# Performance work log

Hardware: AMD Instinct MI355X
Metric: run time of the kernel (lower is better)

The kernel has to match this reference:

```python
import jax, jax.numpy as jnp
import numpy as np

DIM, FFN, GC, NSET, K = 48, 2, 2, 32, 3
HID = DIM * FFN          # 96 hidden features
G = HID // GC            # 48 groups in KBA
CG = HID // G            # 2 channels per group
INTERC = 24              # min(dim, 24)
B, H, W = 4, 128, 128


def _conv(x, w, b=None, groups=1, pad=0):
    out = jax.lax.conv_general_dilated(
        x, w, (1, 1), [(pad, pad), (pad, pad)],
        dimension_numbers=('NCHW', 'OIHW', 'NCHW'),
        feature_group_count=groups)
    if b is not None:
        out = out + b[None, :, None, None]
    return out


def _kba(x, att, k, g, bb, ww):
    # x: [B,c,H,W], att: [B,nset,H,W], bb: [1,nset,c], ww: [1,nset,c*c//g*k*k]
    Bz, c, Hh, Ww = x.shape
    KK = k * k
    cg = c // g
    P = Hh * Ww
    a = att.reshape(Bz, -1, P).transpose(0, 2, 1)                     # [B,P,nset]
    bias = jnp.einsum('bpn,nc->bpc', a, bb[0])                        # [B,P,c]
    attk = jnp.einsum('bpn,nm->bpm', a, ww[0]).reshape(Bz, P, g, cg, cg * KK)
    pd = k // 2
    xp = jnp.pad(x, ((0, 0), (0, 0), (pd, pd), (pd, pd)))
    # im2col patches, torch.unfold layout: channel-major, kernel row-major
    patches = jnp.stack([xp[:, :, i:i + Hh, j:j + Ww]
                         for i in range(k) for j in range(k)], axis=2)  # [B,c,KK,H,W]
    uf = patches.reshape(Bz, g, cg * KK, P).transpose(0, 3, 1, 2)       # [B,P,g,cg*KK]
    out = jnp.einsum('bpgom,bpgm->bpgo', attk, uf).reshape(Bz, P, c) + bias
    return out.transpose(0, 2, 1).reshape(Bz, c, Hh, Ww)


def setup_inputs() -> dict:
    key = jax.random.key(0)
    ks = jax.random.split(key, 20)
    s = 0.05
    inp = {
        'x': jax.random.normal(ks[0], (B, DIM, H, W), jnp.float32),
        'dw1_w': jax.random.normal(ks[1], (HID, DIM, 1, 1), jnp.float32) * s,
        'dw2_w': jax.random.normal(ks[2], (HID, 1, 3, 3), jnp.float32) * s,
        'proj_w': jax.random.normal(ks[3], (DIM, HID, 1, 1), jnp.float32) * s,
        'sca_w': jax.random.normal(ks[4], (HID, HID, 1, 1), jnp.float32) * s,
        'sca_b': jax.random.normal(ks[5], (HID,), jnp.float32) * s,
        'c1_w1': jax.random.normal(ks[6], (HID, DIM, 1, 1), jnp.float32) * s,
        'c1_w2': jax.random.normal(ks[7], (HID, 1, 3, 3), jnp.float32) * s,
        'kba_w': jax.random.normal(ks[8], (1, NSET, HID * CG * K * K), jnp.float32) * s,
        'kba_b': jax.random.normal(ks[9], (1, NSET, HID), jnp.float32) * s,
        'c2_w1': jax.random.normal(ks[10], (INTERC, DIM // INTERC, 3, 3), jnp.float32) * s,
        'c2_b1': jax.random.normal(ks[11], (INTERC,), jnp.float32) * s,
        'c2_w2': jax.random.normal(ks[12], (NSET, INTERC // 2, 1, 1), jnp.float32) * s,
        'c2_b2': jax.random.normal(ks[13], (NSET,), jnp.float32) * s,
        'c211_w': jax.random.normal(ks[14], (NSET, DIM, 1, 1), jnp.float32) * s,
        'c211_b': jax.random.normal(ks[15], (NSET,), jnp.float32) * s,
        'attgamma': jnp.full((1, NSET, 1, 1), 0.01, jnp.float32),
        'ga1': jnp.full((1, HID, 1, 1), 0.01, jnp.float32),
    }
    return inp


def reference(x, dw1_w, dw2_w, proj_w, sca_w, sca_b, c1_w1, c1_w2,
              kba_w, kba_b, c2_w1, c2_b1, c2_w2, c2_b2,
              c211_w, c211_b, attgamma, ga1):
    # dwconv branch: 1x1 -> depthwise 3x3
    x1 = _conv(_conv(x, dw1_w), dw2_w, groups=HID, pad=1)
    # attention map branch: grouped 3x3 -> SimpleGate -> 1x1, scaled + skip 1x1
    t = _conv(x, c2_w1, c2_b1, groups=INTERC, pad=1)
    t1, t2 = jnp.split(t, 2, axis=1)
    t = _conv(t1 * t2, c2_w2, c2_b2)
    att = t * attgamma + _conv(x, c211_w, c211_b)
    # conv1 branch feeding KBA
    uf = _conv(_conv(x, c1_w1), c1_w2, groups=HID, pad=1)
    x2 = _kba(uf, att, K, G, kba_b, kba_w) * ga1 + uf
    comb = jax.nn.gelu(x1, approximate=False) * x2
    pooled = jnp.mean(comb, axis=(2, 3), keepdims=True)
    comb = comb * _conv(pooled, sca_w, sca_b)
    return _conv(comb, proj_w)
```

## Files before the change

kernel.cpp:

```cpp
#include <hip/hip_runtime.h>
#include <math.h>

#define BB 4
#define HH 128
#define WW 128
#define HWP (HH*WW)
#define DIMC 48
#define HIDC 96
#define NSETC 32

typedef __attribute__((ext_vector_type(8))) short bf16x8;
typedef __attribute__((ext_vector_type(4))) float f32x4;
typedef __attribute__((ext_vector_type(2))) float f32x2;

static __device__ __forceinline__ unsigned short f2bf(float f) {
    union { float f; unsigned u; } v; v.f = f;
    unsigned r = (v.u + 0x7FFFu + ((v.u >> 16) & 1u)) >> 16;
    return (unsigned short)r;
}
static __device__ __forceinline__ unsigned rnd_bf(float f) {
    union { float f; unsigned u; } v; v.f = f;
    return v.u + 0x8000u;
}
static __device__ __forceinline__ unsigned pack2bf(float lo, float hi) {
    return __builtin_amdgcn_perm(rnd_bf(hi), rnd_bf(lo), 0x07060302u);
}
static __device__ __forceinline__ void st_bf_hi(unsigned short* p, float f) {
    *p = (unsigned short)(rnd_bf(f) >> 16);
}
static __device__ __forceinline__ float bf2f(unsigned short u) {
    union { unsigned u; float f; } v; v.u = ((unsigned)u) << 16;
    return v.f;
}
static __device__ __forceinline__ float bfpair_lo(unsigned pr) {
    union { unsigned u; float f; } v; v.u = pr << 16; return v.f;
}
static __device__ __forceinline__ float bfpair_hi(unsigned pr) {
    union { unsigned u; float f; } v; v.u = pr & 0xffff0000u; return v.f;
}
static __device__ __forceinline__ float gelu(float x) {
    return 0.5f * x * (1.0f + erff(x * 0.70710678118654752f));
}

__global__ __launch_bounds__(256) void k_prep(
    const float* __restrict__ x,
    const float* __restrict__ kbaw, const float* __restrict__ kbab,
    const float* __restrict__ dw1w, const float* __restrict__ c1w1,
    const float* __restrict__ ga1,  const float* __restrict__ c211w,
    const float* __restrict__ c2w2, const float* __restrict__ c2b2,
    const float* __restrict__ c211b, const float* __restrict__ attg,
    unsigned short* __restrict__ Bpk, unsigned short* __restrict__ Bpw,
    unsigned short* __restrict__ Aps, unsigned short* __restrict__ Ag,
    unsigned* __restrict__ x_p, float* __restrict__ pooled)
{
    __shared__ unsigned ts[256 * 26];
    int blk = blockIdx.x, tid = threadIdx.x;
    if (blk < 300) {
        int t = blk * 256 + tid;
        if (t < 61440) {
            int j = t & 7, lane = (t >> 3) & 63, tile = t >> 9;
            int chunk = tile / 10, nt = tile - chunk * 10;
            int m = lane & 15, qn = lane >> 4;
            int lc = 4 * nt + (m & 3);
            int o = lc / 20, tt = lc % 20;
            int c = (m >> 2) * 24 + 2 * chunk + o;
            int n = qn * 8 + j;
            float v = 0.f;
            if (tt < 18)       v = kbaw[n * 1728 + (c >> 1) * 36 + (c & 1) * 18 + tt] * ga1[c];
            else if (tt == 18) v = kbab[n * 96 + c] * ga1[c];
            Bpk[t] = f2bf(v);
        } else if (t < 73728) {
            int u = t - 61440;
            int s = u / 6144;
            int rem = u % 6144;
            int nt = rem >> 9;
            int lane = (rem >> 3) & 63, j = rem & 7;
            int k = s * 32 + ((lane >> 4) << 3) + j;
            int col = (nt << 4) + (lane & 15);
            float v = 0.f;
            if (k < 48) v = (col < 96) ? dw1w[col * 48 + k] : c1w1[(col - 96) * 48 + k];
            Bpw[u] = f2bf(v);
        } else if (t < 75776) {
            int u = t - 73728;
            int j = u & 7, lane = (u >> 3) & 63, tile = u >> 9;
            int kt = tile >> 1, nt2 = tile & 1;
            int m = lane & 15, qn = lane >> 4;
            int n = 8 * (m >> 2) + 4 * nt2 + (m & 3);
            int k = kt * 32 + qn * 8 + j;
            Aps[u] = f2bf(k < 48 ? c211w[n * 48 + k] : 0.f);
        } else if (t < 76800) {
            int u = t - 75776;
            int j = u & 7, lane = (u >> 3) & 63, nt2 = u >> 9;
            int m = lane & 15, qn = lane >> 4;
            int n = 8 * (m >> 2) + 4 * nt2 + (m & 3);
            int k = qn * 8 + j;
            float v = 0.f;
            if (k < 12)       v = c2w2[n * 12 + k] * attg[n];
            else if (k == 12) v = c2b2[n] * attg[n] + c211b[n];
            Ag[u] = f2bf(v);
        }
    } else {
        int xblk = blk - 300;
        if (xblk == 0) {
            for (int i = tid; i < BB * HIDC; i += 256) pooled[i] = 0.f;
        }
        int b = xblk >> 6;
        int p0 = (xblk & 63) << 8;
        const float* xb = x + (size_t)b * DIMC * HWP + p0;
        #pragma unroll
        for (int c2 = 0; c2 < 24; ++c2) {
            float lo = xb[(2 * c2) * HWP + tid];
            float hi = xb[(2 * c2 + 1) * HWP + tid];
            ts[tid * 26 + c2] = pack2bf(lo, hi);
        }
        __syncthreads();
        unsigned* dst = x_p + ((size_t)b * HWP + p0) * 24;
        for (int idx = tid; idx < 256 * 24; idx += 256) {
            int px = idx / 24, j2 = idx - px * 24;
            dst[px * 24 + j2] = ts[px * 26 + j2];
        }
    }
}

__global__ __launch_bounds__(256, 2) void k_mff(
    const unsigned* __restrict__ x_p,
    const uint4* __restrict__ BpkA, const uint4* __restrict__ Bpw,
    const uint4* __restrict__ Aps,  const uint4* __restrict__ Ag,
    const float* __restrict__ c1w2, const float* __restrict__ dw2w,
    const float* __restrict__ c2w1, const float* __restrict__ c2b1,
    unsigned* __restrict__ comb_bf, float* __restrict__ pooled)
{
    __shared__ __attribute__((aligned(16))) unsigned xs[144 * 26];
    __shared__ __attribute__((aligned(16))) unsigned short hsw[144 * 100];
    __shared__ unsigned short us2p[100 * 100];
    __shared__ float wls[864 + 432 + 24];
    __shared__ float pooled_s[96];

    int lane = threadIdx.x, wy = threadIdx.y;
    int tid = wy * 64 + lane;
    int blk = blockIdx.x;
    int b = blk >> 8, ty = (blk >> 4) & 15, tx = blk & 15;
    int q = lane >> 4, i16 = lane & 15;

    float* wats  = wls + 864;
    float* c2b1s = wls + 864 + 432;
    float* att_tf = (float*)hsw;

    if (tid < 96) pooled_s[tid] = 0.f;
    for (int idx = tid; idx < 864; idx += 256) {
        int t5 = idx / 96, c = idx - t5 * 96;
        wls[idx] = dw2w[c * 9 + t5];
    }
    for (int idx = tid; idx < 216; idx += 256) {
        int g = idx / 9, tap = idx - g * 9;
        wats[idx * 2]     = c2w1[g * 18 + tap];
        wats[idx * 2 + 1] = c2w1[g * 18 + 9 + tap];
    }
    if (tid < 24) c2b1s[tid] = c2b1[tid];
    for (int idx = tid; idx < 144 * 12; idx += 256) {
        int pos = idx / 12, jp = idx - pos * 12;
        int gy = ty * 8 - 2 + pos / 12, gx = tx * 8 - 2 + pos % 12;
        uint2 v = {0u, 0u};
        if (((unsigned)gy < (unsigned)HH) & ((unsigned)gx < (unsigned)WW))
            v = *(const uint2*)&x_p[((size_t)b * HWP + gy * WW + gx) * 24 + jp * 2];
        *(uint2*)&xs[pos * 26 + jp * 2] = v;
    }
    __syncthreads();

    int p_t = wy * 16 + i16;
    int pyT = p_t >> 3, pxT = p_t & 7;
    int gp = (ty * 8 + pyT) * WW + tx * 8 + pxT;
    uint4 z4 = {0u, 0u, 0u, 0u};

    #pragma unroll
    for (int ci = 0; ci < 6; ++ci) {
        int g = q * 6 + ci;
        float acc = c2b1s[g];
        #pragma unroll
        for (int di = 0; di < 3; ++di)
          #pragma unroll
          for (int dj = 0; dj < 3; ++dj) {
              unsigned pr = xs[((pyT + 1 + di) * 12 + pxT + 1 + dj) * 26 + g];
              f32x2 w2 = *(const f32x2*)&wats[(g * 9 + di * 3 + dj) * 2];
              acc += w2.x * bfpair_lo(pr) + w2.y * bfpair_hi(pr);
          }
        att_tf[p_t * 26 + g] = acc;
    }
    __syncthreads();

    bf16x8 afrag;
    {
        int p26 = p_t * 26;
        unsigned tgd[4];
        #pragma unroll
        for (int i2 = 0; i2 < 4; ++i2) {
            int k0 = q * 8 + 2 * i2;
            int k1 = k0 + 1;
            float v0 = (k0 < 12) ? att_tf[p26 + k0] * att_tf[p26 + 12 + k0] : (k0 == 12 ? 1.f : 0.f);
            float v1 = (k1 < 12) ? att_tf[p26 + k1] * att_tf[p26 + 12 + k1] : (k1 == 12 ? 1.f : 0.f);
            tgd[i2] = pack2bf(v0, v1);
        }
        uint4 tgr = {tgd[0], tgd[1], tgd[2], tgd[3]};
        bf16x8 btg = __builtin_bit_cast(bf16x8, tgr);

        int cen = (pyT + 2) * 12 + (pxT + 2);
        uint2 xa = *(const uint2*)&xs[cen * 26 + q * 4];
        uint2 xb2 = *(const uint2*)&xs[cen * 26 + q * 4 + 2];
        uint4 bx0r = {xa.x, xa.y, xb2.x, xb2.y};
        uint4 bx1r = z4;
        if (q < 2) {
            uint2 xc = *(const uint2*)&xs[cen * 26 + 16 + q * 4];
            uint2 xd = *(const uint2*)&xs[cen * 26 + 16 + q * 4 + 2];
            bx1r.x = xc.x; bx1r.y = xc.y; bx1r.z = xd.x; bx1r.w = xd.y;
        }
        bf16x8 bx0 = __builtin_bit_cast(bf16x8, bx0r);
        bf16x8 bx1 = __builtin_bit_cast(bf16x8, bx1r);

        float attv[8];
        #pragma unroll
        for (int nt2 = 0; nt2 < 2; ++nt2) {
            bf16x8 ag  = __builtin_bit_cast(bf16x8, Ag[nt2 * 64 + lane]);
            bf16x8 as0 = __builtin_bit_cast(bf16x8, Aps[nt2 * 64 + lane]);
            bf16x8 as1 = __builtin_bit_cast(bf16x8, Aps[(2 + nt2) * 64 + lane]);
            f32x4 z = {0.f, 0.f, 0.f, 0.f};
            f32x4 c = __builtin_amdgcn_mfma_f32_16x16x32_bf16(ag, btg, z, 0, 0, 0);
            c = __builtin_amdgcn_mfma_f32_16x16x32_bf16(as1, bx1, c, 0, 0, 0);
            c = __builtin_amdgcn_mfma_f32_16x16x32_bf16(as0, bx0, c, 0, 0, 0);
            #pragma unroll
            for (int r = 0; r < 4; ++r) attv[nt2 * 4 + r] = c[r];
        }
        uint4 au = {pack2bf(attv[0], attv[1]), pack2bf(attv[2], attv[3]),
                    pack2bf(attv[4], attv[5]), pack2bf(attv[6], attv[7])};
        afrag = __builtin_bit_cast(bf16x8, au);
    }
    __syncthreads();

    {
        int rgA[3]; int nA;
        if (wy == 0) { rgA[0] = 0; rgA[1] = 4; rgA[2] = 8; nA = 3; }
        else         { rgA[0] = wy; rgA[1] = wy + 4; rgA[2] = 0; nA = 2; }
        #pragma unroll 1
        for (int rr = 0; rr < nA; ++rr) {
            int rg = rgA[rr];
            int hp = rg * 16 + i16;
            uint2 xa = *(const uint2*)&xs[hp * 26 + q * 4];
            uint2 xb2 = *(const uint2*)&xs[hp * 26 + q * 4 + 2];
            uint4 a0r = {xa.x, xa.y, xb2.x, xb2.y};
            uint4 a1r = z4;
            if (q < 2) {
                uint2 xc = *(const uint2*)&xs[hp * 26 + 16 + q * 4];
                uint2 xd = *(const uint2*)&xs[hp * 26 + 16 + q * 4 + 2];
                a1r.x = xc.x; a1r.y = xc.y; a1r.z = xd.x; a1r.w = xd.y;
            }
            bf16x8 a0 = __builtin_bit_cast(bf16x8, a0r);
            bf16x8 a1 = __builtin_bit_cast(bf16x8, a1r);
            int rowb = rg * 16 + 4 * q;
            #pragma unroll
            for (int nt = 0; nt < 6; ++nt) {
                bf16x8 b0 = __builtin_bit_cast(bf16x8, Bpw[(size_t)((6 + nt) << 6) + lane]);
                bf16x8 b1 = __builtin_bit_cast(bf16x8, Bpw[(size_t)((18 + nt) << 6) + lane]);
                f32x4 z = {0.f, 0.f, 0.f, 0.f};
                f32x4 c = __builtin_amdgcn_mfma_f32_16x16x32_bf16(a1, b1, z, 0, 0, 0);
                c = __builtin_amdgcn_mfma_f32_16x16x32_bf16(a0, b0, c, 0, 0, 0);
                #pragma unroll
                for (int r = 0; r < 4; ++r)
                    st_bf_hi(&hsw[(rowb + r) * 100 + nt * 16 + i16], c[r]);
            }
        }
    }
    __syncthreads();

    #pragma unroll 1
    for (int ci = 0; ci < 3; ++ci) {
        int cq = wy * 3 + ci;
        const float* w9 = c1w2 + cq * 8 * 9;
        #pragma unroll 1
        for (int sub = 0; sub < 2; ++sub) {
            int hp2 = sub * 64 + lane;
            if (hp2 < 100) {
                int py2 = hp2 / 10, px2 = hp2 - py2 * 10;
                float acc[8];
                #pragma unroll
                for (int c = 0; c < 8; ++c) acc[c] = 0.f;
                #pragma unroll
                for (int di = 0; di < 3; ++di)
                  #pragma unroll
                  for (int dj = 0; dj < 3; ++dj) {
                      int row = (py2 + di) * 12 + px2 + dj;
                      uint2 v0 = *(const uint2*)&hsw[row * 100 + cq * 8];
                      uint2 v1 = *(const uint2*)&hsw[row * 100 + cq * 8 + 4];
                      unsigned pp[4] = {v0.x, v0.y, v1.x, v1.y};
                      #pragma unroll
                      for (int c2 = 0; c2 < 4; ++c2) {
                          acc[2*c2]   += w9[(2*c2) * 9 + di * 3 + dj]   * bfpair_lo(pp[c2]);
                          acc[2*c2+1] += w9[(2*c2+1) * 9 + di * 3 + dj] * bfpair_hi(pp[c2]);
                      }
                  }
                uint2 o0, o1;
                o0.x = pack2bf(acc[0], acc[1]);
                o0.y = pack2bf(acc[2], acc[3]);
                o1.x = pack2bf(acc[4], acc[5]);
                o1.y = pack2bf(acc[6], acc[7]);
                *(uint2*)&us2p[hp2 * 100 + cq * 8]     = o0;
                *(uint2*)&us2p[hp2 * 100 + cq * 8 + 4] = o1;
            }
        }
    }
    __syncthreads();

    {
        int rgB[2]; rgB[0] = wy; rgB[1] = wy + 4;
        int nB = (wy < 3) ? 2 : 1;
        #pragma unroll 1
        for (int rr = 0; rr < nB; ++rr) {
            int rg = rgB[rr];
            int hp = rg * 16 + i16;
            bool okp = hp < 100;
            int hy = hp / 10, hx = hp - hy * 10;
            int pos = okp ? ((hy + 1) * 12 + hx + 1) : 0;
            uint2 xa = *(const uint2*)&xs[pos * 26 + q * 4];
            uint2 xb2 = *(const uint2*)&xs[pos * 26 + q * 4 + 2];
            uint4 a0r = {xa.x, xa.y, xb2.x, xb2.y};
            uint4 a1r = z4;
            if (q < 2) {
                uint2 xc = *(const uint2*)&xs[pos * 26 + 16 + q * 4];
                uint2 xd = *(const uint2*)&xs[pos * 26 + 16 + q * 4 + 2];
                a1r.x = xc.x; a1r.y = xc.y; a1r.z = xd.x; a1r.w = xd.y;
            }
            bf16x8 a0 = __builtin_bit_cast(bf16x8, a0r);
            bf16x8 a1 = __builtin_bit_cast(bf16x8, a1r);
            int rowb = rg * 16 + 4 * q;
            #pragma unroll
            for (int nt = 0; nt < 6; ++nt) {
                bf16x8 b0 = __builtin_bit_cast(bf16x8, Bpw[(size_t)(nt << 6) + lane]);
                bf16x8 b1 = __builtin_bit_cast(bf16x8, Bpw[(size_t)((12 + nt) << 6) + lane]);
                f32x4 z = {0.f, 0.f, 0.f, 0.f};
                f32x4 c = __builtin_amdgcn_mfma_f32_16x16x32_bf16(a1, b1, z, 0, 0, 0);
                c = __builtin_amdgcn_mfma_f32_16x16x32_bf16(a0, b0, c, 0, 0, 0);
                #pragma unroll
                for (int r = 0; r < 4; ++r)
                    st_bf_hi(&hsw[(rowb + r) * 100 + nt * 16 + i16], c[r]);
            }
        }
    }
    __syncthreads();

    f32x2 greg[12];
    {
        int base = q * 24;
        #pragma unroll
        for (int cc = 0; cc < 12; ++cc) {
            int c0 = base + 2 * cc;
            f32x2 acc = {0.f, 0.f};
            #pragma unroll
            for (int di = 0; di < 3; ++di)
              #pragma unroll
              for (int dj = 0; dj < 3; ++dj) {
                  unsigned pr = *(const unsigned*)&hsw[((pyT + di) * 10 + pxT + dj) * 100 + c0];
                  f32x2 hv = {bfpair_lo(pr), bfpair_hi(pr)};
                  f32x2 wv = *(const f32x2*)&wls[(di * 3 + dj) * 96 + c0];
                  acc += wv * hv;
              }
            greg[cc].x = gelu(acc.x);
            greg[cc].y = gelu(acc.y);
        }
    }

    unsigned* cmb = comb_bf + ((size_t)b * HWP + gp) * 48 + q * 12;
    int hpC = (pyT + 1) * 10 + pxT + 1;

    #pragma unroll
    for (int chunk = 0; chunk < 12; ++chunk) {
        f32x4 cf[10];
        #pragma unroll
        for (int nt = 0; nt < 10; ++nt) {
            bf16x8 aW = __builtin_bit_cast(bf16x8, BpkA[(size_t)((chunk * 10 + nt) << 6) + lane]);
            f32x4 z = {0.f, 0.f, 0.f, 0.f};
            cf[nt] = __builtin_amdgcn_mfma_f32_16x16x32_bf16(aW, afrag, z, 0, 0, 0);
        }
        int c0 = q * 24 + 2 * chunk;
        float u[18];
        #pragma unroll
        for (int i = 0; i < 3; ++i)
          #pragma unroll
          for (int j = 0; j < 3; ++j) {
              unsigned pr = *(const unsigned*)&us2p[((pyT + i) * 10 + pxT + j) * 100 + c0];
              u[i * 3 + j]     = bfpair_lo(pr);
              u[9 + i * 3 + j] = bfpair_hi(pr);
          }
        float acc0 = cf[4][2];
        float acc1 = cf[9][2];
        #pragma unroll
        for (int m = 0; m < 16; ++m) {
            acc0 += cf[m >> 2][m & 3]       * u[m];
            acc1 += cf[5 + (m >> 2)][m & 3] * u[m];
        }
        acc0 += cf[4][0] * u[16] + cf[4][1] * u[17];
        acc1 += cf[9][0] * u[16] + cf[9][1] * u[17];

        unsigned sp = *(const unsigned*)&us2p[hpC * 100 + c0];
        float x20 = acc0 + bfpair_lo(sp);
        float x21 = acc1 + bfpair_hi(sp);
        float cv0 = greg[chunk].x * x20;
        float cv1 = greg[chunk].y * x21;
        cmb[chunk] = pack2bf(cv0, cv1);
        float r0 = cv0, r1 = cv1;
        #pragma unroll
        for (int s = 1; s < 16; s <<= 1) {
            r0 += __shfl_xor(r0, s, 64);
            r1 += __shfl_xor(r1, s, 64);
        }
        if (i16 == 0) {
            atomicAdd(&pooled_s[c0], r0);
            atomicAdd(&pooled_s[c0 + 1], r1);
        }
    }
    __syncthreads();
    if (tid < 96) atomicAdd(&pooled[b * HIDC + tid], pooled_s[tid]);
}

__global__ __launch_bounds__(256) void k_final(
    const unsigned* __restrict__ comb_bf, const float* __restrict__ pooled,
    const float* __restrict__ scaw, const float* __restrict__ scab,
    const float* __restrict__ projw, float* __restrict__ out)
{
    __shared__ float svs[96];
    __shared__ float cs[96][66];
    int tid = threadIdx.x;
    int blk = blockIdx.x;
    int p0 = blk * 64;
    int b = p0 >> 14;
    if (tid < 96) {
        float dot = 0.f;
        const float* pr = pooled + b * 96;
        const float* wr = scaw + tid * 96;
        #pragma unroll 4
        for (int k = 0; k < 96; ++k) dot += wr[k] * pr[k];
        svs[tid] = scab[tid] + dot * (1.0f / (float)HWP);
    }
    __syncthreads();
    for (int idx = tid; idx < 64 * 12; idx += 256) {
        int px = idx / 12, cq = idx - px * 12;
        uint4 v = *(const uint4*)&comb_bf[(size_t)(p0 + px) * 48 + cq * 4];
        int k0 = cq * 8;
        unsigned pp[4] = {v.x, v.y, v.z, v.w};
        #pragma unroll
        for (int j = 0; j < 4; ++j) {
            cs[k0 + 2*j][px]     = bfpair_lo(pp[j]) * svs[k0 + 2*j];
            cs[k0 + 2*j + 1][px] = bfpair_hi(pp[j]) * svs[k0 + 2*j + 1];
        }
    }
    __syncthreads();
    int l = tid & 63, w = tid >> 6;
    int o0 = w * 12;
    float acc[12];
    #pragma unroll
    for (int o = 0; o < 12; ++o) acc[o] = 0.f;
    #pragma unroll 4
    for (int k = 0; k < 96; ++k) {
        float v = cs[k][l];
        #pragma unroll
        for (int o = 0; o < 12; ++o)
            acc[o] += projw[(o0 + o) * 96 + k] * v;
    }
    float* ob = out + (size_t)b * DIMC * HWP + (p0 & 16383) + l;
    #pragma unroll
    for (int o = 0; o < 12; ++o)
        ob[(o0 + o) * HWP] = acc[o];
}

extern "C" void kernel_launch(void* const* d_in, const int* in_sizes, int n_in,
                              void* d_out, int out_size, void* d_ws, size_t ws_size,
                              hipStream_t stream)
{
    const float* x     = (const float*)d_in[0];
    const float* dw1w  = (const float*)d_in[1];
    const float* dw2w  = (const float*)d_in[2];
    const float* projw = (const float*)d_in[3];
    const float* scaw  = (const float*)d_in[4];
    const float* scab  = (const float*)d_in[5];
    const float* c1w1  = (const float*)d_in[6];
    const float* c1w2  = (const float*)d_in[7];
    const float* kbaw  = (const float*)d_in[8];
    const float* kbab  = (const float*)d_in[9];
    const float* c2w1  = (const float*)d_in[10];
    const float* c2b1  = (const float*)d_in[11];
    const float* c2w2  = (const float*)d_in[12];
    const float* c2b2  = (const float*)d_in[13];
    const float* c211w = (const float*)d_in[14];
    const float* c211b = (const float*)d_in[15];
    const float* attg  = (const float*)d_in[16];
    const float* ga1   = (const float*)d_in[17];

    unsigned* x_p     = (unsigned*)d_ws;
    unsigned* comb_bf = x_p + (size_t)BB * HWP * 24;
    float* pooled     = (float*)(comb_bf + (size_t)BB * HWP * 48);
    unsigned short* BpkA = (unsigned short*)(pooled + BB * HIDC);
    unsigned short* Bpw  = BpkA + 61440;
    unsigned short* Aps  = Bpw + 12288;
    unsigned short* Ag   = Aps + 2048;

    k_prep <<<556,  256, 0, stream>>>(x, kbaw, kbab, dw1w, c1w1, ga1, c211w, c2w2, c2b2,
                                      c211b, attg, BpkA, Bpw, Aps, Ag, x_p, pooled);
    k_mff  <<<1024, dim3(64,4,1), 0, stream>>>(x_p, (const uint4*)BpkA, (const uint4*)Bpw,
                                               (const uint4*)Aps, (const uint4*)Ag,
                                               c1w2, dw2w, c2w1, c2b1, comb_bf, pooled);
    k_final<<<1024, 256, 0, stream>>>(comb_bf, pooled, scaw, scab, projw, (float*)d_out);
}
```

Measured before the change: 208.9 us.

## Double k_mff block to eight waves and split channel and tap work across them

The fused k_mff kernel now runs 512 threads (8 waves) per block instead of 256. Each stage's work is split across the extra waves: attention grouped-conv channels, 1x1 MFMA row groups, depthwise-conv subtiles, and the gelu and KBA chunks are divided by channel half and pixel group. The intent is more waves in flight per CU to hide LDS and MFMA latency, and a shorter serial chain per wave. In exchange, the launch bounds of (512,4) squeeze the per-thread register budget, which risks spills given the large MFMA accumulator arrays. Shared memory use also limits how many blocks can actually be resident, and some att/afrag work is duplicated across waves.

```diff
diff --git a/kernel.cpp b/kernel.cpp
--- a/kernel.cpp
+++ b/kernel.cpp
@@ -122,7 +122,7 @@
     }
 }
 
-__global__ __launch_bounds__(256, 2) void k_mff(
+__global__ __launch_bounds__(512, 4) void k_mff(
     const unsigned* __restrict__ x_p,
     const uint4* __restrict__ BpkA, const uint4* __restrict__ Bpw,
     const uint4* __restrict__ Aps,  const uint4* __restrict__ Ag,
@@ -141,23 +141,25 @@
     int blk = blockIdx.x;
     int b = blk >> 8, ty = (blk >> 4) & 15, tx = blk & 15;
     int q = lane >> 4, i16 = lane & 15;
+    int wh = wy >> 2;
+    int wp = wy & 3;
 
     float* wats  = wls + 864;
     float* c2b1s = wls + 864 + 432;
     float* att_tf = (float*)hsw;
 
     if (tid < 96) pooled_s[tid] = 0.f;
-    for (int idx = tid; idx < 864; idx += 256) {
+    for (int idx = tid; idx < 864; idx += 512) {
         int t5 = idx / 96, c = idx - t5 * 96;
         wls[idx] = dw2w[c * 9 + t5];
     }
-    for (int idx = tid; idx < 216; idx += 256) {
+    for (int idx = tid; idx < 216; idx += 512) {
         int g = idx / 9, tap = idx - g * 9;
         wats[idx * 2]     = c2w1[g * 18 + tap];
         wats[idx * 2 + 1] = c2w1[g * 18 + 9 + tap];
     }
     if (tid < 24) c2b1s[tid] = c2b1[tid];
-    for (int idx = tid; idx < 144 * 12; idx += 256) {
+    for (int idx = tid; idx < 144 * 12; idx += 512) {
         int pos = idx / 12, jp = idx - pos * 12;
         int gy = ty * 8 - 2 + pos / 12, gx = tx * 8 - 2 + pos % 12;
         uint2 v = {0u, 0u};
@@ -167,14 +169,14 @@
     }
     __syncthreads();
 
-    int p_t = wy * 16 + i16;
+    int p_t = wp * 16 + i16;
     int pyT = p_t >> 3, pxT = p_t & 7;
     int gp = (ty * 8 + pyT) * WW + tx * 8 + pxT;
     uint4 z4 = {0u, 0u, 0u, 0u};
 
     #pragma unroll
-    for (int ci = 0; ci < 6; ++ci) {
-        int g = q * 6 + ci;
+    for (int ci = 0; ci < 3; ++ci) {
+        int g = q * 6 + wh * 3 + ci;
         float acc = c2b1s[g];
         #pragma unroll
         for (int di = 0; di < 3; ++di)
@@ -236,12 +238,10 @@
     __syncthreads();
 
     {
-        int rgA[3]; int nA;
-        if (wy == 0) { rgA[0] = 0; rgA[1] = 4; rgA[2] = 8; nA = 3; }
-        else         { rgA[0] = wy; rgA[1] = wy + 4; rgA[2] = 0; nA = 2; }
+        int nA = (wy == 0) ? 2 : 1;
         #pragma unroll 1
         for (int rr = 0; rr < nA; ++rr) {
-            int rg = rgA[rr];
+            int rg = rr ? 8 : wy;
             int hp = rg * 16 + i16;
             uint2 xa = *(const uint2*)&xs[hp * 26 + q * 4];
             uint2 xb2 = *(const uint2*)&xs[hp * 26 + q * 4 + 2];
@@ -271,85 +271,78 @@
     __syncthreads();
 
     #pragma unroll 1
-    for (int ci = 0; ci < 3; ++ci) {
-        int cq = wy * 3 + ci;
+    for (int it = 0; it < 3; ++it) {
+        int su = wy * 3 + it;
+        int cq = su >> 1;
         const float* w9 = c1w2 + cq * 8 * 9;
-        #pragma unroll 1
-        for (int sub = 0; sub < 2; ++sub) {
-            int hp2 = sub * 64 + lane;
-            if (hp2 < 100) {
-                int py2 = hp2 / 10, px2 = hp2 - py2 * 10;
-                float acc[8];
-                #pragma unroll
-                for (int c = 0; c < 8; ++c) acc[c] = 0.f;
-                #pragma unroll
-                for (int di = 0; di < 3; ++di)
+        int hp2 = (su & 1) * 50 + lane;
+        if (lane < 50) {
+            int py2 = hp2 / 10, px2 = hp2 - py2 * 10;
+            float acc[8];
+            #pragma unroll
+            for (int c = 0; c < 8; ++c) acc[c] = 0.f;
+            #pragma unroll
+            for (int di = 0; di < 3; ++di)
+              #pragma unroll
+              for (int dj = 0; dj < 3; ++dj) {
+                  int row = (py2 + di) * 12 + px2 + dj;
+                  uint2 v0 = *(const uint2*)&hsw[row * 100 + cq * 8];
+                  uint2 v1 = *(const uint2*)&hsw[row * 100 + cq * 8 + 4];
+                  unsigned pp[4] = {v0.x, v0.y, v1.x, v1.y};
                   #pragma unroll
-                  for (int dj = 0; dj < 3; ++dj) {
-                      int row = (py2 + di) * 12 + px2 + dj;
-                      uint2 v0 = *(const uint2*)&hsw[row * 100 + cq * 8];
-                      uint2 v1 = *(const uint2*)&hsw[row * 100 + cq * 8 + 4];
-                      unsigned pp[4] = {v0.x, v0.y, v1.x, v1.y};
-                      #pragma unroll
-                      for (int c2 = 0; c2 < 4; ++c2) {
-                          acc[2*c2]   += w9[(2*c2) * 9 + di * 3 + dj]   * bfpair_lo(pp[c2]);
-                          acc[2*c2+1] += w9[(2*c2+1) * 9 + di * 3 + dj] * bfpair_hi(pp[c2]);
-                      }
+                  for (int c2 = 0; c2 < 4; ++c2) {
+                      acc[2*c2]   += w9[(2*c2) * 9 + di * 3 + dj]   * bfpair_lo(pp[c2]);
+                      acc[2*c2+1] += w9[(2*c2+1) * 9 + di * 3 + dj] * bfpair_hi(pp[c2]);
                   }
-                uint2 o0, o1;
-                o0.x = pack2bf(acc[0], acc[1]);
-                o0.y = pack2bf(acc[2], acc[3]);
-                o1.x = pack2bf(acc[4], acc[5]);
-                o1.y = pack2bf(acc[6], acc[7]);
-                *(uint2*)&us2p[hp2 * 100 + cq * 8]     = o0;
-                *(uint2*)&us2p[hp2 * 100 + cq * 8 + 4] = o1;
-            }
-        }
-    }
-    __syncthreads();
-
+              }
+            uint2 o0, o1;
+            o0.x = pack2bf(acc[0], acc[1]);
+            o0.y = pack2bf(acc[2], acc[3]);
+            o1.x = pack2bf(acc[4], acc[5]);
+            o1.y = pack2bf(acc[6], acc[7]);
+            *(uint2*)&us2p[hp2 * 100 + cq * 8]     = o0;
+            *(uint2*)&us2p[hp2 * 100 + cq * 8 + 4] = o1;
+        }
+    }
+    __syncthreads();
+
+    if (wy < 7) {
+        int rg = wy;
+        int hp = rg * 16 + i16;
+        bool okp = hp < 100;
+        int hy = hp / 10, hx = hp - hy * 10;
+        int pos = okp ? ((hy + 1) * 12 + hx + 1) : 0;
+        uint2 xa = *(const uint2*)&xs[pos * 26 + q * 4];
+        uint2 xb2 = *(const uint2*)&xs[pos * 26 + q * 4 + 2];
+        uint4 a0r = {xa.x, xa.y, xb2.x, xb2.y};
+        uint4 a1r = z4;
+        if (q < 2) {
+            uint2 xc = *(const uint2*)&xs[pos * 26 + 16 + q * 4];
+            uint2 xd = *(const uint2*)&xs[pos * 26 + 16 + q * 4 + 2];
+            a1r.x = xc.x; a1r.y = xc.y; a1r.z = xd.x; a1r.w = xd.y;
+        }
+        bf16x8 a0 = __builtin_bit_cast(bf16x8, a0r);
+        bf16x8 a1 = __builtin_bit_cast(bf16x8, a1r);
+        int rowb = rg * 16 + 4 * q;
+        #pragma unroll
+        for (int nt = 0; nt < 6; ++nt) {
+            bf16x8 b0 = __builtin_bit_cast(bf16x8, Bpw[(size_t)(nt << 6) + lane]);
+            bf16x8 b1 = __builtin_bit_cast(bf16x8, Bpw[(size_t)((12 + nt) << 6) + lane]);
+            f32x4 z = {0.f, 0.f, 0.f, 0.f};
+            f32x4 c = __builtin_amdgcn_mfma_f32_16x16x32_bf16(a1, b1, z, 0, 0, 0);
+            c = __builtin_amdgcn_mfma_f32_16x16x32_bf16(a0, b0, c, 0, 0, 0);
+            #pragma unroll
+            for (int r = 0; r < 4; ++r)
+                st_bf_hi(&hsw[(rowb + r) * 100 + nt * 16 + i16], c[r]);
+        }
+    }
+    __syncthreads();
+
+    f32x2 greg[6];
     {
-        int rgB[2]; rgB[0] = wy; rgB[1] = wy + 4;
-        int nB = (wy < 3) ? 2 : 1;
-        #pragma unroll 1
-        for (int rr = 0; rr < nB; ++rr) {
-            int rg = rgB[rr];
-            int hp = rg * 16 + i16;
-            bool okp = hp < 100;
-            int hy = hp / 10, hx = hp - hy * 10;
-            int pos = okp ? ((hy + 1) * 12 + hx + 1) : 0;
-            uint2 xa = *(const uint2*)&xs[pos * 26 + q * 4];
-            uint2 xb2 = *(const uint2*)&xs[pos * 26 + q * 4 + 2];
-            uint4 a0r = {xa.x, xa.y, xb2.x, xb2.y};
-            uint4 a1r = z4;
-            if (q < 2) {
-                uint2 xc = *(const uint2*)&xs[pos * 26 + 16 + q * 4];
-                uint2 xd = *(const uint2*)&xs[pos * 26 + 16 + q * 4 + 2];
-                a1r.x = xc.x; a1r.y = xc.y; a1r.z = xd.x; a1r.w = xd.y;
-            }
-            bf16x8 a0 = __builtin_bit_cast(bf16x8, a0r);
-            bf16x8 a1 = __builtin_bit_cast(bf16x8, a1r);
-            int rowb = rg * 16 + 4 * q;
-            #pragma unroll
-            for (int nt = 0; nt < 6; ++nt) {
-                bf16x8 b0 = __builtin_bit_cast(bf16x8, Bpw[(size_t)(nt << 6) + lane]);
-                bf16x8 b1 = __builtin_bit_cast(bf16x8, Bpw[(size_t)((12 + nt) << 6) + lane]);
-                f32x4 z = {0.f, 0.f, 0.f, 0.f};
-                f32x4 c = __builtin_amdgcn_mfma_f32_16x16x32_bf16(a1, b1, z, 0, 0, 0);
-                c = __builtin_amdgcn_mfma_f32_16x16x32_bf16(a0, b0, c, 0, 0, 0);
-                #pragma unroll
-                for (int r = 0; r < 4; ++r)
-                    st_bf_hi(&hsw[(rowb + r) * 100 + nt * 16 + i16], c[r]);
-            }
-        }
-    }
-    __syncthreads();
-
-    f32x2 greg[12];
-    {
-        int base = q * 24;
-        #pragma unroll
-        for (int cc = 0; cc < 12; ++cc) {
+        int base = q * 24 + wh * 12;
+        #pragma unroll
+        for (int cc = 0; cc < 6; ++cc) {
             int c0 = base + 2 * cc;
             f32x2 acc = {0.f, 0.f};
             #pragma unroll
@@ -370,7 +363,8 @@
     int hpC = (pyT + 1) * 10 + pxT + 1;
 
     #pragma unroll
-    for (int chunk = 0; chunk < 12; ++chunk) {
+    for (int cl = 0; cl < 6; ++cl) {
+        int chunk = wh * 6 + cl;
         f32x4 cf[10];
         #pragma unroll
         for (int nt = 0; nt < 10; ++nt) {
@@ -401,8 +395,8 @@
         unsigned sp = *(const unsigned*)&us2p[hpC * 100 + c0];
         float x20 = acc0 + bfpair_lo(sp);
         float x21 = acc1 + bfpair_hi(sp);
-        float cv0 = greg[chunk].x * x20;
-        float cv1 = greg[chunk].y * x21;
+        float cv0 = greg[cl].x * x20;
+        float cv1 = greg[cl].y * x21;
         cmb[chunk] = pack2bf(cv0, cv1);
         float r0 = cv0, r1 = cv1;
         #pragma unroll
@@ -502,7 +496,7 @@
 
     k_prep <<<556,  256, 0, stream>>>(x, kbaw, kbab, dw1w, c1w1, ga1, c211w, c2w2, c2b2,
                                       c211b, attg, BpkA, Bpw, Aps, Ag, x_p, pooled);
-    k_mff  <<<1024, dim3(64,4,1), 0, stream>>>(x_p, (const uint4*)BpkA, (const uint4*)Bpw,
+    k_mff  <<<1024, dim3(64,8,1), 0, stream>>>(x_p, (const uint4*)BpkA, (const uint4*)Bpw,
                                                (const uint4*)Aps, (const uint4*)Ag,
                                                c1w2, dw2w, c2w1, c2b1, comb_bf, pooled);
     k_final<<<1024, 256, 0, stream>>>(comb_bf, pooled, scaw, scab, projw, (float*)d_out);
```

Measured after the change: 206.1 us. No clear change (-1.4%).
